# Performance work log

Measured on AMD Instinct MI355X. Metric: run time of the kernel, lower is better.

The kernel has to match this reference:

```python
import jax, jax.numpy as jnp
import numpy as np

K = 512          # num_embeddings
D = 64           # embedding_dim
BETA = 0.25      # commitment_cost
DECAY = 0.99
EPS = 1e-5


def setup_inputs() -> dict:
    key = jax.random.key(0)
    k1, k2, k3 = jax.random.split(key, 3)
    inputs = jax.random.normal(k1, (64, D, 32, 32), dtype=jnp.float32)  # NCHW, C == embedding_dim
    embedding = jax.random.normal(k2, (K, D), dtype=jnp.float32)
    ema_w = jax.random.normal(k3, (K, D), dtype=jnp.float32)
    ema_cluster_size = jnp.zeros((K,), dtype=jnp.float32)
    return {"inputs": inputs, "embedding": embedding, "ema_w": ema_w,
            "ema_cluster_size": ema_cluster_size}


def reference(inputs, embedding, ema_w, ema_cluster_size):
    # NCHW -> NHWC, flatten to [N, D]
    x = jnp.transpose(inputs, (0, 2, 3, 1))
    B, H, W, C = x.shape
    flat = x.reshape(-1, C)                                   # [N, D]

    # squared L2 distances to all codes: [N, K]
    d = (jnp.sum(flat * flat, axis=1, keepdims=True)
         + jnp.sum(embedding * embedding, axis=1)
         - 2.0 * flat @ embedding.T)
    idx = jnp.argmin(d, axis=1)                               # [N]

    # gather (equivalent to one-hot @ embedding, without materializing one-hot)
    quantized = embedding[idx].reshape(x.shape)               # [B,H,W,D]

    # EMA codebook update (training branch); segment sums replace encodings.T matmuls
    counts = jax.ops.segment_sum(jnp.ones_like(idx, dtype=flat.dtype), idx,
                                 num_segments=K)              # [K]
    new_cs = ema_cluster_size * DECAY + (1.0 - DECAY) * counts
    n = jnp.sum(new_cs)
    new_cs = (new_cs + EPS) / (n + K * EPS) * n               # Laplace smoothing
    dw = jax.ops.segment_sum(flat, idx, num_segments=K)       # [K, D]
    new_ema_w = ema_w * DECAY + (1.0 - DECAY) * dw
    new_embedding = new_ema_w / new_cs[:, None]

    # commitment loss + straight-through estimator
    e_latent_loss = jnp.mean((jax.lax.stop_gradient(quantized) - x) ** 2)
    loss = BETA * e_latent_loss
    quantized_st = x + jax.lax.stop_gradient(quantized - x)

    avg_probs = counts / flat.shape[0]
    perplexity = jnp.exp(-jnp.sum(avg_probs * jnp.log(avg_probs + 1e-10)))

    out_q = jnp.transpose(quantized_st, (0, 3, 1, 2))         # back to NCHW
    return (loss, out_q, perplexity, idx.reshape(B, H, W),
            new_cs, new_ema_w, new_embedding)
```

## Files before the change

kernel.cpp:

```cpp
#include <hip/hip_runtime.h>

#define K_CODES 512
#define DIM 64
#define HW 1024
#define NVEC 65536
#define NREP 8

#define O0 0
#define O1 1
#define O2 4194305
#define O3 4194306
#define O4 4259842
#define O5 4260354
#define O6 4293122

#define WS_EE   0
#define WS_CNT  512
#define WS_LOSS 4608
#define WS_N    6656
#define WS_DW   6912
#define WS_BP   269056

typedef __bf16 bf16x8 __attribute__((ext_vector_type(8)));
typedef float  f32x4  __attribute__((ext_vector_type(4)));

union U2 { unsigned int u; unsigned short us[2]; __bf16 h[2]; };

__global__ void k0_init(const float* __restrict__ emb, const float* __restrict__ ema_cs,
                        float* __restrict__ wsf) {
    __shared__ float sn[256];
    const int b = blockIdx.x, t = threadIdx.x;
    if (b < 128) {
        #pragma unroll
        for (int i = 0; i < 8; ++i)
            wsf[WS_DW + b * 2048 + i * 256 + t] = 0.0f;
    } else if (b == 128) {
        int* cnt = (int*)(wsf + WS_CNT);
        #pragma unroll
        for (int i = 0; i < 16; ++i) cnt[i * 256 + t] = 0;
        sn[t] = ema_cs[t] + ema_cs[t + 256];
        __syncthreads();
        for (int s = 128; s > 0; s >>= 1) {
            if (t < s) sn[t] += sn[t + s];
            __syncthreads();
        }
        if (t == 0) wsf[WS_N] = 0.99f * sn[0] + 0.01f * 65536.0f;
    } else if (b < 131) {
        int k = (b - 129) * 256 + t;
        const float* e = emb + k * DIM;
        float s = 0.0f;
        #pragma unroll
        for (int c = 0; c < DIM; ++c) s += e[c] * e[c];
        wsf[WS_EE + k] = s;
    } else {
        int g = (b - 131) * 256 + t;
        int j    = g & 7;
        int lane = (g >> 3) & 63;
        int ks   = (g >> 9) & 1;
        int rest = g >> 10;
        int ntg  = rest & 31;
        int s    = rest >> 5;
        int code = ntg * 16 + (lane & 15);
        int c    = ks * 32 + (lane >> 4) * 8 + j;
        float v = -2.0f * emb[code * DIM + c];
        __bf16 h0 = (__bf16)v;  float r1 = v  - (float)h0;
        __bf16 h1 = (__bf16)r1; float r2 = r1 - (float)h1;
        __bf16 hv = (s == 0) ? h0 : (s == 1 ? h1 : (__bf16)r2);
        ((__bf16*)(wsf + WS_BP))[g] = hv;
    }
}

__global__ __launch_bounds__(256, 4)
void k1_main(const float* __restrict__ in, const float* __restrict__ emb,
             float* __restrict__ out, float* __restrict__ wsf) {
    __shared__ unsigned int xsp[3][32 * 36];
    __shared__ float xxp[32][9];
    __shared__ float pmin[4][32];
    __shared__ int   pidx[4][32];
    __shared__ float xxs[32];
    __shared__ int   hist[K_CODES];

    const int t    = threadIdx.x;
    const int lane = t & 63;
    const int wave = t >> 6;
    const int ni   = wave;
    const int col  = lane & 15;
    const int quad = lane >> 4;

    hist[t] = 0; hist[t + 256] = 0;

    const int blk     = blockIdx.x;
    const int rep     = blk & (NREP - 1);
    const int n_img   = blk >> 5;
    const int hw_base = (blk & 31) * 32;
    const float* xbase = in + n_img * (DIM * HW) + hw_base;

    f32x4 acc[2][8];
    #pragma unroll
    for (int nt = 0; nt < 8; ++nt) {
        float eev = wsf[WS_EE + ni * 128 + nt * 16 + col];
        #pragma unroll
        for (int mi = 0; mi < 2; ++mi) {
            acc[mi][nt][0] = eev; acc[mi][nt][1] = eev;
            acc[mi][nt][2] = eev; acc[mi][nt][3] = eev;
        }
    }

    {
        const int h   = t & 31;
        const int cp0 = t >> 5;
        float xxa = 0.0f;
        #pragma unroll
        for (int it = 0; it < 4; ++it) {
            int cp = it * 8 + cp0;
            float v0 = xbase[(2 * cp) * HW + h];
            float v1 = xbase[(2 * cp + 1) * HW + h];
            __bf16 a0 = (__bf16)v0; float ra = v0 - (float)a0;
            __bf16 a1 = (__bf16)ra; ra -= (float)a1;
            __bf16 a2 = (__bf16)ra;
            __bf16 b0 = (__bf16)v1; float rb = v1 - (float)b0;
            __bf16 b1 = (__bf16)rb; rb -= (float)b1;
            __bf16 b2 = (__bf16)rb;
            U2 u0, u1, u2;
            u0.h[0] = a0; u0.h[1] = b0;
            u1.h[0] = a1; u1.h[1] = b1;
            u2.h[0] = a2; u2.h[1] = b2;
            xsp[0][h * 36 + cp] = u0.u;
            xsp[1][h * 36 + cp] = u1.u;
            xsp[2][h * 36 + cp] = u2.u;
            xxa += v0 * v0 + v1 * v1;
        }
        xxp[h][cp0] = xxa;
    }
    __syncthreads();

    if (t < 32) {
        float s = 0.0f;
        #pragma unroll
        for (int j = 0; j < 8; ++j) s += xxp[t][j];
        xxs[t] = s;
    }

    const bf16x8* bp8 = (const bf16x8*)(wsf + WS_BP);

    #pragma unroll
    for (int ks = 0; ks < 2; ++ks) {
        bf16x8 A0[2], A1[2], A2[2];
        #pragma unroll
        for (int mi = 0; mi < 2; ++mi) {
            int u = (mi * 16 + col) * 36 + ks * 16 + quad * 4;
            A0[mi] = *(const bf16x8*)&xsp[0][u];
            A1[mi] = *(const bf16x8*)&xsp[1][u];
            A2[mi] = *(const bf16x8*)&xsp[2][u];
        }
        #pragma unroll
        for (int s = 0; s < 3; ++s) {
            #pragma unroll
            for (int bh = 0; bh < 2; ++bh) {
                bf16x8 Bv[4];
                #pragma unroll
                for (int n4 = 0; n4 < 4; ++n4) {
                    int nt = bh * 4 + n4;
                    Bv[n4] = bp8[(((s * 32 + ni * 8 + nt) * 2 + ks) * 64) + lane];
                }
                #pragma unroll
                for (int mi = 0; mi < 2; ++mi)
                    #pragma unroll
                    for (int n4 = 0; n4 < 4; ++n4)
                        acc[mi][bh * 4 + n4] = __builtin_amdgcn_mfma_f32_16x16x32_bf16(A0[mi], Bv[n4], acc[mi][bh * 4 + n4], 0, 0, 0);
                if (s < 2) {
                    #pragma unroll
                    for (int mi = 0; mi < 2; ++mi)
                        #pragma unroll
                        for (int n4 = 0; n4 < 4; ++n4)
                            acc[mi][bh * 4 + n4] = __builtin_amdgcn_mfma_f32_16x16x32_bf16(A1[mi], Bv[n4], acc[mi][bh * 4 + n4], 0, 0, 0);
                }
                if (s == 0) {
                    #pragma unroll
                    for (int mi = 0; mi < 2; ++mi)
                        #pragma unroll
                        for (int n4 = 0; n4 < 4; ++n4)
                            acc[mi][bh * 4 + n4] = __builtin_amdgcn_mfma_f32_16x16x32_bf16(A2[mi], Bv[n4], acc[mi][bh * 4 + n4], 0, 0, 0);
                }
            }
        }
    }

    #pragma unroll
    for (int mi = 0; mi < 2; ++mi) {
        #pragma unroll
        for (int r = 0; r < 4; ++r) {
            float v  = acc[mi][0][r];
            int   bi = ni * 128 + col;
            #pragma unroll
            for (int nt = 1; nt < 8; ++nt) {
                float u  = acc[mi][nt][r];
                int   ui = ni * 128 + nt * 16 + col;
                if (u < v) { v = u; bi = ui; }
            }
            #pragma unroll
            for (int off = 1; off < 16; off <<= 1) {
                float ov = __shfl_xor(v, off);
                int   oi = __shfl_xor(bi, off);
                if (ov < v || (ov == v && oi < bi)) { v = ov; bi = oi; }
            }
            if (col == 0) {
                int row = mi * 16 + quad * 4 + r;
                pmin[ni][row] = v;
                pidx[ni][row] = bi;
            }
        }
    }
    __syncthreads();

    if (t < 32) {
        float v = pmin[0][t]; int bi = pidx[0][t];
        #pragma unroll
        for (int q = 1; q < 4; ++q) {
            float u = pmin[q][t]; int ui = pidx[q][t];
            if (u < v) { v = u; bi = ui; }
        }
        pidx[0][t] = bi;
        out[O3 + blk * 32 + t] = (float)bi;
        atomicAdd(&hist[bi], 1);
        float ld = v + xxs[t];
        #pragma unroll
        for (int off = 16; off > 0; off >>= 1) ld += __shfl_down(ld, off);
        if (t == 0) wsf[WS_LOSS + blk] = ld;
    }
    __syncthreads();

    {
        int v = t & 31, cq = t >> 5;
        int kv = pidx[0][v];
        const float* ew = emb + kv * DIM;
        float* oq = out + O1 + n_img * (DIM * HW) + hw_base + v;
        #pragma unroll
        for (int c = cq * 8; c < cq * 8 + 8; ++c) oq[c * HW] = ew[c];
    }

    {
        float* dwr = wsf + WS_DW + rep * 32768;
        #pragma unroll 1
        for (int v8 = 0; v8 < 8; ++v8) {
            int v  = wave * 8 + v8;
            int kv = pidx[0][v];
            int wi = v * 36 + (lane >> 1);
            U2 a0, a1, a2;
            a0.u = xsp[0][wi]; a1.u = xsp[1][wi]; a2.u = xsp[2][wi];
            int hs = lane & 1;
            float val = (float)a0.h[hs] + (float)a1.h[hs] + (float)a2.h[hs];
            atomicAdd(&dwr[kv * 64 + lane], val);
        }
    }

    int* cnt = (int*)(wsf + WS_CNT);
    if (hist[t])       atomicAdd(&cnt[rep * 512 + t], hist[t]);
    if (hist[t + 256]) atomicAdd(&cnt[rep * 512 + t + 256], hist[t + 256]);
}

__global__ void k2(const float* __restrict__ ema_cs, const float* __restrict__ ema_w,
                   float* __restrict__ out, const float* __restrict__ wsf) {
    __shared__ float s1[256], s2[256];
    const int t = threadIdx.x;
    const int blk = blockIdx.x;
    const int* cnt = (const int*)(wsf + WS_CNT);

    if (blk == 128) {
        float ls = 0.0f;
        #pragma unroll
        for (int j = 0; j < 8; ++j) ls += wsf[WS_LOSS + j * 256 + t];
        s1[t] = ls;
        float ca = 0.0f, cb = 0.0f;
        #pragma unroll
        for (int r = 0; r < NREP; ++r) {
            ca += (float)cnt[r * 512 + t];
            cb += (float)cnt[r * 512 + 256 + t];
        }
        float pa = ca * (1.0f / 65536.0f);
        float pb = cb * (1.0f / 65536.0f);
        s2[t] = pa * logf(pa + 1e-10f) + pb * logf(pb + 1e-10f);
        __syncthreads();
        for (int s = 128; s > 0; s >>= 1) {
            if (t < s) { s1[t] += s1[t + s]; s2[t] += s2[t + s]; }
            __syncthreads();
        }
        if (t == 0) {
            out[O0] = 0.25f * s1[0] * (1.0f / 4194304.0f);
            out[O2] = expf(-s2[0]);
        }
        return;
    }

    const int m = blk * 256 + t;
    const int k = m >> 6;
    float ck = 0.0f, dwsum = 0.0f;
    #pragma unroll
    for (int r = 0; r < NREP; ++r) {
        ck    += (float)cnt[r * 512 + k];
        dwsum += wsf[WS_DW + r * 32768 + m];
    }
    float n    = wsf[WS_N];
    float rawk = 0.99f * ema_cs[k] + 0.01f * ck;
    float csk  = (rawk + 1e-5f) / (n + 512.0f * 1e-5f) * n;
    float wv   = 0.99f * ema_w[m] + 0.01f * dwsum;
    out[O5 + m] = wv;
    out[O6 + m] = wv / csk;
    if ((m & 63) == 0) out[O4 + k] = csk;
}

extern "C" void kernel_launch(void* const* d_in, const int* in_sizes, int n_in,
                              void* d_out, int out_size, void* d_ws, size_t ws_size,
                              hipStream_t stream) {
    const float* in     = (const float*)d_in[0];
    const float* emb    = (const float*)d_in[1];
    const float* ema_w  = (const float*)d_in[2];
    const float* ema_cs = (const float*)d_in[3];
    float* out = (float*)d_out;
    float* wsf = (float*)d_ws;

    hipLaunchKernelGGL(k0_init, dim3(515),  dim3(256), 0, stream, emb, ema_cs, wsf);
    hipLaunchKernelGGL(k1_main, dim3(2048), dim3(256), 0, stream, in, emb, out, wsf);
    hipLaunchKernelGGL(k2,      dim3(129),  dim3(256), 0, stream, ema_cs, ema_w, out, wsf);
}
```

Measured before the change: 139.0 us.

## Software-pipeline codebook B-fragment loads across MFMA phases with triple buffering

Restructures the MFMA loop into 12 flattened phases. The codebook B fragments are prefetched two phases ahead into a three-slot register ring, and the first two slots are issued before the barrier, so global load latency overlaps the matrix math. All A fragments are loaded from shared memory up front, and the dw atomic loop is now fully unrolled. The cost is higher register pressure, which could reduce occupancy or cause spills.

```diff
diff --git a/kernel.cpp b/kernel.cpp
--- a/kernel.cpp
+++ b/kernel.cpp
@@ -132,6 +132,17 @@
         }
         xxp[h][cp0] = xxa;
     }
+
+    const bf16x8* bp8 = (const bf16x8*)(wsf + WS_BP);
+
+    bf16x8 Bp[3][4];
+    #pragma unroll
+    for (int n4 = 0; n4 < 4; ++n4)
+        Bp[0][n4] = bp8[(((0 * 32 + ni * 8 + 0 * 4 + n4) * 2 + 0) * 64) + lane];
+    #pragma unroll
+    for (int n4 = 0; n4 < 4; ++n4)
+        Bp[1][n4] = bp8[(((0 * 32 + ni * 8 + 1 * 4 + n4) * 2 + 0) * 64) + lane];
+
     __syncthreads();
 
     if (t < 32) {
@@ -141,48 +152,48 @@
         xxs[t] = s;
     }
 
-    const bf16x8* bp8 = (const bf16x8*)(wsf + WS_BP);
-
-    #pragma unroll
-    for (int ks = 0; ks < 2; ++ks) {
-        bf16x8 A0[2], A1[2], A2[2];
+    bf16x8 Af[2][3][2];
+    #pragma unroll
+    for (int ks = 0; ks < 2; ++ks)
         #pragma unroll
         for (int mi = 0; mi < 2; ++mi) {
             int u = (mi * 16 + col) * 36 + ks * 16 + quad * 4;
-            A0[mi] = *(const bf16x8*)&xsp[0][u];
-            A1[mi] = *(const bf16x8*)&xsp[1][u];
-            A2[mi] = *(const bf16x8*)&xsp[2][u];
-        }
-        #pragma unroll
-        for (int s = 0; s < 3; ++s) {
-            #pragma unroll
-            for (int bh = 0; bh < 2; ++bh) {
-                bf16x8 Bv[4];
+            Af[ks][0][mi] = *(const bf16x8*)&xsp[0][u];
+            Af[ks][1][mi] = *(const bf16x8*)&xsp[1][u];
+            Af[ks][2][mi] = *(const bf16x8*)&xsp[2][u];
+        }
+
+    #pragma unroll
+    for (int p = 0; p < 12; ++p) {
+        const int ks = p / 6, s = (p % 6) / 2, bh = p & 1;
+        if (p < 10) {
+            const int pn = p + 2;
+            const int ksn = pn / 6, sn = (pn % 6) / 2, bhn = pn & 1;
+            #pragma unroll
+            for (int n4 = 0; n4 < 4; ++n4)
+                Bp[pn % 3][n4] = bp8[(((sn * 32 + ni * 8 + bhn * 4 + n4) * 2 + ksn) * 64) + lane];
+        }
+        #pragma unroll
+        for (int mi = 0; mi < 2; ++mi)
+            #pragma unroll
+            for (int n4 = 0; n4 < 4; ++n4)
+                acc[mi][bh * 4 + n4] = __builtin_amdgcn_mfma_f32_16x16x32_bf16(
+                    Af[ks][0][mi], Bp[p % 3][n4], acc[mi][bh * 4 + n4], 0, 0, 0);
+        if (s < 2) {
+            #pragma unroll
+            for (int mi = 0; mi < 2; ++mi)
                 #pragma unroll
-                for (int n4 = 0; n4 < 4; ++n4) {
-                    int nt = bh * 4 + n4;
-                    Bv[n4] = bp8[(((s * 32 + ni * 8 + nt) * 2 + ks) * 64) + lane];
-                }
+                for (int n4 = 0; n4 < 4; ++n4)
+                    acc[mi][bh * 4 + n4] = __builtin_amdgcn_mfma_f32_16x16x32_bf16(
+                        Af[ks][1][mi], Bp[p % 3][n4], acc[mi][bh * 4 + n4], 0, 0, 0);
+        }
+        if (s == 0) {
+            #pragma unroll
+            for (int mi = 0; mi < 2; ++mi)
                 #pragma unroll
-                for (int mi = 0; mi < 2; ++mi)
-                    #pragma unroll
-                    for (int n4 = 0; n4 < 4; ++n4)
-                        acc[mi][bh * 4 + n4] = __builtin_amdgcn_mfma_f32_16x16x32_bf16(A0[mi], Bv[n4], acc[mi][bh * 4 + n4], 0, 0, 0);
-                if (s < 2) {
-                    #pragma unroll
-                    for (int mi = 0; mi < 2; ++mi)
-                        #pragma unroll
-                        for (int n4 = 0; n4 < 4; ++n4)
-                            acc[mi][bh * 4 + n4] = __builtin_amdgcn_mfma_f32_16x16x32_bf16(A1[mi], Bv[n4], acc[mi][bh * 4 + n4], 0, 0, 0);
-                }
-                if (s == 0) {
-                    #pragma unroll
-                    for (int mi = 0; mi < 2; ++mi)
-                        #pragma unroll
-                        for (int n4 = 0; n4 < 4; ++n4)
-                            acc[mi][bh * 4 + n4] = __builtin_amdgcn_mfma_f32_16x16x32_bf16(A2[mi], Bv[n4], acc[mi][bh * 4 + n4], 0, 0, 0);
-                }
-            }
+                for (int n4 = 0; n4 < 4; ++n4)
+                    acc[mi][bh * 4 + n4] = __builtin_amdgcn_mfma_f32_16x16x32_bf16(
+                        Af[ks][2][mi], Bp[p % 3][n4], acc[mi][bh * 4 + n4], 0, 0, 0);
         }
     }
 
@@ -241,7 +252,7 @@
 
     {
         float* dwr = wsf + WS_DW + rep * 32768;
-        #pragma unroll 1
+        #pragma unroll
         for (int v8 = 0; v8 < 8; ++v8) {
             int v  = wave * 8 + v8;
             int kv = pidx[0][v];
```

New measurement: 138.7 us. Within noise of the previous version (-0.3%).

## Fuse epilogue into main kernel via atomic ticket and last-blocks spin-wait

Applied to the files above, without the earlier changes.

Merges the separate finalisation kernel into the main quantization kernel. Each block takes an atomic ticket; the last 129 blocks spin until every tile has finished, then compute the EMA updates, loss and perplexity. This removes one kernel launch and its inter-kernel gap, at the cost of spinning blocks and dependence on all earlier blocks being scheduled. The init kernel also spreads zeroing over more blocks, and the dw scatter loop is unrolled.

```diff
diff --git a/kernel.cpp b/kernel.cpp
--- a/kernel.cpp
+++ b/kernel.cpp
@@ -5,6 +5,8 @@
 #define HW 1024
 #define NVEC 65536
 #define NREP 8
+#define NTILES 2048
+#define NEPI 129
 
 #define O0 0
 #define O1 1
@@ -18,6 +20,7 @@
 #define WS_CNT  512
 #define WS_LOSS 4608
 #define WS_N    6656
+#define WS_DONE 6784
 #define WS_DW   6912
 #define WS_BP   269056
 
@@ -30,14 +33,15 @@
                         float* __restrict__ wsf) {
     __shared__ float sn[256];
     const int b = blockIdx.x, t = threadIdx.x;
-    if (b < 128) {
-        #pragma unroll
-        for (int i = 0; i < 8; ++i)
-            wsf[WS_DW + b * 2048 + i * 256 + t] = 0.0f;
-    } else if (b == 128) {
+    if (b < 256) {
+        #pragma unroll
+        for (int i = 0; i < 4; ++i)
+            wsf[WS_DW + b * 1024 + i * 256 + t] = 0.0f;
+    } else if (b == 256) {
         int* cnt = (int*)(wsf + WS_CNT);
         #pragma unroll
         for (int i = 0; i < 16; ++i) cnt[i * 256 + t] = 0;
+        if (t == 0) *(int*)(wsf + WS_DONE) = 0;
         sn[t] = ema_cs[t] + ema_cs[t + 256];
         __syncthreads();
         for (int s = 128; s > 0; s >>= 1) {
@@ -45,23 +49,23 @@
             __syncthreads();
         }
         if (t == 0) wsf[WS_N] = 0.99f * sn[0] + 0.01f * 65536.0f;
-    } else if (b < 131) {
-        int k = (b - 129) * 256 + t;
+    } else if (b < 259) {
+        int k = (b - 257) * 256 + t;
         const float* e = emb + k * DIM;
         float s = 0.0f;
         #pragma unroll
         for (int c = 0; c < DIM; ++c) s += e[c] * e[c];
         wsf[WS_EE + k] = s;
     } else {
-        int g = (b - 131) * 256 + t;
+        int g = (b - 259) * 256 + t;
         int j    = g & 7;
-        int lane = (g >> 3) & 63;
+        int ln   = (g >> 3) & 63;
         int ks   = (g >> 9) & 1;
         int rest = g >> 10;
         int ntg  = rest & 31;
         int s    = rest >> 5;
-        int code = ntg * 16 + (lane & 15);
-        int c    = ks * 32 + (lane >> 4) * 8 + j;
+        int code = ntg * 16 + (ln & 15);
+        int c    = ks * 32 + (ln >> 4) * 8 + j;
         float v = -2.0f * emb[code * DIM + c];
         __bf16 h0 = (__bf16)v;  float r1 = v  - (float)h0;
         __bf16 h1 = (__bf16)r1; float r2 = r1 - (float)h1;
@@ -71,14 +75,17 @@
 }
 
 __global__ __launch_bounds__(256, 4)
-void k1_main(const float* __restrict__ in, const float* __restrict__ emb,
-             float* __restrict__ out, float* __restrict__ wsf) {
+void kfused(const float* __restrict__ in, const float* __restrict__ emb,
+            const float* __restrict__ ema_w, const float* __restrict__ ema_cs,
+            float* __restrict__ out, float* __restrict__ wsf) {
     __shared__ unsigned int xsp[3][32 * 36];
     __shared__ float xxp[32][9];
     __shared__ float pmin[4][32];
     __shared__ int   pidx[4][32];
     __shared__ float xxs[32];
     __shared__ int   hist[K_CODES];
+    __shared__ float s1[256], s2[256];
+    __shared__ int   sticket;
 
     const int t    = threadIdx.x;
     const int lane = t & 63;
@@ -86,13 +93,15 @@
     const int ni   = wave;
     const int col  = lane & 15;
     const int quad = lane >> 4;
+    const int h    = t & 31;
+    const int cp0  = t >> 5;
 
     hist[t] = 0; hist[t + 256] = 0;
 
-    const int blk     = blockIdx.x;
-    const int rep     = blk & (NREP - 1);
-    const int n_img   = blk >> 5;
-    const int hw_base = (blk & 31) * 32;
+    const int tile    = blockIdx.x;
+    const int rep     = tile & (NREP - 1);
+    const int n_img   = tile >> 5;
+    const int hw_base = (tile & 31) * 32;
     const float* xbase = in + n_img * (DIM * HW) + hw_base;
 
     f32x4 acc[2][8];
@@ -107,8 +116,6 @@
     }
 
     {
-        const int h   = t & 31;
-        const int cp0 = t >> 5;
         float xxa = 0.0f;
         #pragma unroll
         for (int it = 0; it < 4; ++it) {
@@ -221,12 +228,12 @@
             if (u < v) { v = u; bi = ui; }
         }
         pidx[0][t] = bi;
-        out[O3 + blk * 32 + t] = (float)bi;
+        out[O3 + tile * 32 + t] = (float)bi;
         atomicAdd(&hist[bi], 1);
         float ld = v + xxs[t];
         #pragma unroll
         for (int off = 16; off > 0; off >>= 1) ld += __shfl_down(ld, off);
-        if (t == 0) wsf[WS_LOSS + blk] = ld;
+        if (t == 0) wsf[WS_LOSS + tile] = ld;
     }
     __syncthreads();
 
@@ -241,7 +248,7 @@
 
     {
         float* dwr = wsf + WS_DW + rep * 32768;
-        #pragma unroll 1
+        #pragma unroll
         for (int v8 = 0; v8 < 8; ++v8) {
             int v  = wave * 8 + v8;
             int kv = pidx[0][v];
@@ -257,16 +264,25 @@
     int* cnt = (int*)(wsf + WS_CNT);
     if (hist[t])       atomicAdd(&cnt[rep * 512 + t], hist[t]);
     if (hist[t + 256]) atomicAdd(&cnt[rep * 512 + t + 256], hist[t + 256]);
-}
-
-__global__ void k2(const float* __restrict__ ema_cs, const float* __restrict__ ema_w,
-                   float* __restrict__ out, const float* __restrict__ wsf) {
-    __shared__ float s1[256], s2[256];
-    const int t = threadIdx.x;
-    const int blk = blockIdx.x;
-    const int* cnt = (const int*)(wsf + WS_CNT);
-
-    if (blk == 128) {
+
+    __threadfence();
+    __syncthreads();
+    int* done = (int*)(wsf + WS_DONE);
+    if (t == 0) sticket = atomicAdd(done, 1);
+    __syncthreads();
+    const int ticket = sticket;
+    if (ticket < NTILES - NEPI) return;
+
+    if (t == 0) {
+        while (__hip_atomic_load(done, __ATOMIC_ACQUIRE, __HIP_MEMORY_SCOPE_AGENT) < NTILES)
+            __builtin_amdgcn_s_sleep(8);
+    }
+    __syncthreads();
+    __threadfence();
+
+    const int e = ticket - (NTILES - NEPI);
+
+    if (e == 128) {
         float ls = 0.0f;
         #pragma unroll
         for (int j = 0; j < 8; ++j) ls += wsf[WS_LOSS + j * 256 + t];
@@ -292,7 +308,7 @@
         return;
     }
 
-    const int m = blk * 256 + t;
+    const int m = e * 256 + t;
     const int k = m >> 6;
     float ck = 0.0f, dwsum = 0.0f;
     #pragma unroll
@@ -319,7 +335,6 @@
     float* out = (float*)d_out;
     float* wsf = (float*)d_ws;
 
-    hipLaunchKernelGGL(k0_init, dim3(515),  dim3(256), 0, stream, emb, ema_cs, wsf);
-    hipLaunchKernelGGL(k1_main, dim3(2048), dim3(256), 0, stream, in, emb, out, wsf);
-    hipLaunchKernelGGL(k2,      dim3(129),  dim3(256), 0, stream, ema_cs, ema_w, out, wsf);
+    hipLaunchKernelGGL(k0_init, dim3(643),  dim3(256), 0, stream, emb, ema_cs, wsf);
+    hipLaunchKernelGGL(kfused,  dim3(2048), dim3(256), 0, stream, in, emb, ema_w, ema_cs, out, wsf);
 }
```

Result: slower. 360.9 us (+159.7%).
